# Optimization experiments

Hardware: AMD Instinct MI355X
Metric: run time of the kernel (lower is better)

Reference implementation:

```python
import jax, jax.numpy as jnp
import numpy as np

HID, H, HKV, D, INT, S, T = 2048, 16, 8, 128, 6144, 4096, 512
POS = 0          # absolute position of the first token in this prefill chunk
EPS = 1e-6
SCALE = 1.0 / D ** 0.5
REP = H // HKV


def setup_inputs() -> dict:
    key = jax.random.key(0)
    ks = jax.random.split(key, 12)
    w = lambda k, sh: jax.random.normal(k, sh, dtype=jnp.float32) * 0.02

    hidden_conv = jax.random.normal(ks[0], (1, HID, 1, T), dtype=jnp.float32)

    # RoPE tables for absolute positions POS..POS+T-1, HF half-rotation layout
    inv_freq = 1.0 / (10000.0 ** (jnp.arange(0, D, 2, dtype=jnp.float32) / D))
    pos = (POS + jnp.arange(T, dtype=jnp.float32))
    ang = pos[:, None] * inv_freq[None, :]                      # (T, D/2)
    emb = jnp.concatenate([ang, ang], axis=-1)                  # (T, D)
    cos = jnp.cos(emb)[None]                                    # (1, T, D)
    sin = jnp.sin(emb)[None]

    # one-hot write mask: column t has a 1 at row POS+t
    update_mask = jnp.zeros((S, T), jnp.float32).at[POS + jnp.arange(T), jnp.arange(T)].set(1.0)[None, None]
    # causal mask over the cache: slot s visible to token t iff s <= POS+t
    attn_mask = jnp.where(jnp.arange(S)[None, :] <= (POS + jnp.arange(T))[:, None], 0.0, -1e4).astype(jnp.float32)[None, None]

    k_cache = jnp.zeros((1, HKV, S, D), jnp.float32)
    v_cache = jnp.zeros((1, HKV, S, D), jnp.float32)

    return dict(
        hidden_conv=hidden_conv, cos=cos, sin=sin,
        update_mask=update_mask, attn_mask=attn_mask,
        k_cache=k_cache, v_cache=v_cache,
        wq=w(ks[1], (H * D, HID)), wk=w(ks[2], (HKV * D, HID)),
        wv=w(ks[3], (HKV * D, HID)), wo=w(ks[4], (HID, H * D)),
        ln1_w=jnp.ones((HID,), jnp.float32), ln2_w=jnp.ones((HID,), jnp.float32),
        qn_w=jnp.ones((D,), jnp.float32), kn_w=jnp.ones((D,), jnp.float32),
        w_gate_up=w(ks[5], (2 * INT, HID)), w_down=w(ks[6], (HID, INT)),
    )


def _rms(x, w):
    return x * jax.lax.rsqrt(jnp.mean(x * x, axis=-1, keepdims=True) + EPS) * w


def _rotate_half(x):
    x1, x2 = jnp.split(x, 2, axis=-1)
    return jnp.concatenate([-x2, x1], axis=-1)


def reference(hidden_conv, cos, sin, update_mask, attn_mask, k_cache, v_cache,
              wq, wk, wv, wo, ln1_w, ln2_w, qn_w, kn_w, w_gate_up, w_down):
    # (1, HID, 1, T) conv layout -> (1, T, HID)
    x = jnp.transpose(hidden_conv[:, :, 0, :], (0, 2, 1))

    h = _rms(x, ln1_w)
    # 1x1 conv == linear; channel order h*D+d matches view(1,H,D,T)
    q = jnp.einsum('btc,oc->bto', h, wq).reshape(1, T, H, D).transpose(0, 2, 1, 3)    # (1,H,T,D)
    k = jnp.einsum('btc,oc->bto', h, wk).reshape(1, T, HKV, D).transpose(0, 2, 1, 3)  # (1,HKV,T,D)
    v = jnp.einsum('btc,oc->bto', h, wv).reshape(1, T, HKV, D).transpose(0, 2, 1, 3)

    q = _rms(q, qn_w)
    k = _rms(k, kn_w)

    cos_b = cos[:, None]  # (1,1,T,D)
    sin_b = sin[:, None]
    q = q * cos_b + _rotate_half(q) * sin_b
    k = k * cos_b + _rotate_half(k) * sin_b

    # matmul-based KV cache write via one-hot mask (faithful to original)
    k_inc = jnp.matmul(update_mask, k)                 # (1,HKV,S,D)
    v_inc = jnp.matmul(update_mask, v)
    write_any = jnp.sum(update_mask, axis=-1, keepdims=True)  # (1,1,S,1)
    k_full = k_cache * (1.0 - write_any) + k_inc
    v_full = v_cache * (1.0 - write_any) + v_inc

    k_rep = jnp.repeat(k_full, REP, axis=1)            # (1,H,S,D)
    v_rep = jnp.repeat(v_full, REP, axis=1)

    scores = jnp.einsum('bhtd,bhsd->bhts', q, k_rep) * SCALE + attn_mask  # (1,H,T,S)
    attn = jax.nn.softmax(scores, axis=-1)
    out = jnp.einsum('bhts,bhsd->bhtd', attn, v_rep)   # (1,H,T,D)

    o_in = out.transpose(0, 2, 1, 3).reshape(1, T, H * D)
    attn_out = jnp.einsum('btc,oc->bto', o_in, wo)
    hidden = x + attn_out

    h2 = _rms(hidden, ln2_w)
    gate_up = jnp.einsum('btc,oc->bto', h2, w_gate_up)
    gate, up = jnp.split(gate_up, 2, axis=-1)
    mlp = jnp.einsum('bti,oi->bto', jax.nn.silu(gate) * up, w_down)
    hidden = hidden + mlp

    hidden_out = jnp.transpose(hidden, (0, 2, 1))[:, :, None, :]  # back to (1,HID,1,T)
    return hidden_out, k_full, v_full


if __name__ == '__main__':
    outs = reference(**setup_inputs())
    print([o.shape for o in outs])
```

## Files before the change

### kernel.cpp

```cpp
#include <hip/hip_runtime.h>
#include <hip/hip_bf16.h>
#include <hip/hip_fp16.h>

#define TT 512
#define HIDD 2048
#define NH 16
#define NKV 8
#define DD 128
#define INTR 6144
#define SEQ 4096
#define SCALE 0.08838834764831845f

typedef __attribute__((ext_vector_type(8))) short short8;
typedef __attribute__((ext_vector_type(4))) float floatx4;

static __device__ __forceinline__ unsigned short f2b(float f) {
  unsigned int u = __float_as_uint(f);
  u += 0x7fffu + ((u >> 16) & 1u);
  return (unsigned short)(u >> 16);
}

static __device__ __forceinline__ unsigned int f2b2(float a, float b) {
  __hip_bfloat162 h = __float22bfloat162_rn(make_float2(a, b));
  return *reinterpret_cast<unsigned int*>(&h);
}


static __device__ __forceinline__ void gld16(const void* g, void* l) {
  __builtin_amdgcn_global_load_lds(
      (const __attribute__((address_space(1))) unsigned int*)g,
      (__attribute__((address_space(3))) unsigned int*)l, 16, 0, 0);
}

template <int BM, bool B16>
static __device__ __forceinline__ void stage_tile(const unsigned short* __restrict__ A, int lda,
                                                  const void* __restrict__ B, int ldb, int k0,
                                                  unsigned char* buf, int wave, int lane) {
  {
    const int rpw = BM >> 2;
    const int rl = lane >> 2;
    const int c8 = (((lane & 3) ^ ((rl >> 1) & 3)) << 3);
#pragma unroll
    for (int i = 0; i < BM / 64; ++i) {
      const int rbase = wave * rpw + i * 16;
      gld16(A + (size_t)(rbase + rl) * lda + k0 + c8, buf + (size_t)rbase * 64);
    }
  }
  unsigned char* Bb = buf + BM * 64;
  if constexpr (B16) {
    const unsigned short* Bh = (const unsigned short*)B;
    const int rl = lane >> 2;
    const int c8 = (((lane & 3) ^ ((rl >> 1) & 3)) << 3);
#pragma unroll
    for (int i = 0; i < 2; ++i) {
      const int rbase = wave * 32 + i * 16;
      gld16(Bh + (size_t)(rbase + rl) * ldb + k0 + c8, Bb + (size_t)rbase * 64);
    }
  } else {
    const float* Bf = (const float*)B;
    const int rl = lane >> 3;
    const int sp = lane & 7;
#pragma unroll
    for (int i = 0; i < 4; ++i) {
      const int rbase = wave * 32 + i * 8;
      const int r = rbase + rl;
      gld16(Bf + (size_t)r * ldb + k0 + ((sp ^ (r & 7)) << 2), Bb + (size_t)rbase * 128);
    }
  }
}

template <int BM, bool B16>
static __device__ __forceinline__ void frags_from(const unsigned char* buf, int wr, int wc,
                                                  int lrow, int q,
                                                  short8 (&af)[BM / 32], short8 (&bfr)[4]) {
  const int koffA = ((q ^ ((lrow >> 1) & 3)) << 3);
  const unsigned short* Ab = (const unsigned short*)buf;
#pragma unroll
  for (int mi = 0; mi < BM / 32; ++mi)
    af[mi] = *reinterpret_cast<const short8*>(Ab + (size_t)(wr + mi * 16 + lrow) * 32 + koffA);
  if constexpr (B16) {
    const unsigned short* Bb = (const unsigned short*)(buf + BM * 64);
#pragma unroll
    for (int ni = 0; ni < 4; ++ni)
      bfr[ni] = *reinterpret_cast<const short8*>(Bb + (size_t)(wc + ni * 16 + lrow) * 32 + koffA);
  } else {
    const float* Bf = (const float*)(buf + BM * 64);
    const int s0 = q << 1;
#pragma unroll
    for (int ni = 0; ni < 4; ++ni) {
      const int r = wc + ni * 16 + lrow;
      const float4 x = *reinterpret_cast<const float4*>(Bf + (size_t)r * 32 + ((s0 ^ (r & 7)) << 2));
      const float4 y = *reinterpret_cast<const float4*>(Bf + (size_t)r * 32 + (((s0 + 1) ^ (r & 7)) << 2));
      union { short8 s; unsigned int u[4]; } pk;
      pk.u[0] = f2b2(x.x, x.y); pk.u[1] = f2b2(x.z, x.w);
      pk.u[2] = f2b2(y.x, y.y); pk.u[3] = f2b2(y.z, y.w);
      bfr[ni] = pk.s;
    }
  }
}

template <int BM, bool B16>
static __device__ __forceinline__ void gemm_core(const unsigned short* __restrict__ A, int lda,
                                                 const void* __restrict__ B, int ldb,
                                                 int kbeg, int kend, floatx4 (&acc)[BM / 32][4],
                                                 unsigned char* Ls) {
  constexpr int MI = BM / 32;
  constexpr int TILE = BM * 64 + (B16 ? 8192 : 16384);
  constexpr int NB = (BM / 64) + (B16 ? 2 : 4);
  const int tid = threadIdx.x;
  const int lane = tid & 63, wave = tid >> 6;
  const int wr = (wave >> 1) * (BM >> 1);
  const int wc = (wave & 1) << 6;
  const int lrow = lane & 15;
  const int q = lane >> 4;
  const int NT = (kend - kbeg) >> 5;
  stage_tile<BM, B16>(A, lda, B, ldb, kbeg,      Ls,        wave, lane);
  stage_tile<BM, B16>(A, lda, B, ldb, kbeg + 32, Ls + TILE, wave, lane);
  int p = 0;
  for (int t = 0; t < NT - 1; ++t) {
    if constexpr (NB == 6)      asm volatile("s_waitcnt vmcnt(6)" ::: "memory");
    else if constexpr (NB == 3) asm volatile("s_waitcnt vmcnt(3)" ::: "memory");
    else if constexpr (NB == 4) asm volatile("s_waitcnt vmcnt(4)" ::: "memory");
    else                        asm volatile("s_waitcnt vmcnt(5)" ::: "memory");
    __builtin_amdgcn_sched_barrier(0);
    __builtin_amdgcn_s_barrier();
    short8 af[MI], bfr[4];
    frags_from<BM, B16>(Ls + p * TILE, wr, wc, lrow, q, af, bfr);
    asm volatile("s_waitcnt lgkmcnt(0)" ::: "memory");
    __builtin_amdgcn_sched_barrier(0);
    __builtin_amdgcn_s_barrier();
    if (t + 2 < NT)
      stage_tile<BM, B16>(A, lda, B, ldb, kbeg + (t + 2) * 32, Ls + p * TILE, wave, lane);
#pragma unroll
    for (int mi = 0; mi < MI; ++mi)
#pragma unroll
      for (int ni = 0; ni < 4; ++ni)
        acc[mi][ni] = __builtin_amdgcn_mfma_f32_16x16x32_bf16(af[mi], bfr[ni], acc[mi][ni], 0, 0, 0);
    p ^= 1;
  }
  asm volatile("s_waitcnt vmcnt(0)" ::: "memory");
  __builtin_amdgcn_sched_barrier(0);
  __builtin_amdgcn_s_barrier();
  {
    short8 af[MI], bfr[4];
    frags_from<BM, B16>(Ls + p * TILE, wr, wc, lrow, q, af, bfr);
#pragma unroll
    for (int mi = 0; mi < MI; ++mi)
#pragma unroll
      for (int ni = 0; ni < 4; ++ni)
        acc[mi][ni] = __builtin_amdgcn_mfma_f32_16x16x32_bf16(af[mi], bfr[ni], acc[mi][ni], 0, 0, 0);
  }
}

#define EPI_VARS \
  const int lane = threadIdx.x & 63; \
  const int wave = threadIdx.x >> 6; \
  const int wc = (wave & 1) << 6;    \
  const int lrow = lane & 15;        \
  const int quad = lane >> 4;

#define ZERO_ACC(MI_) \
  floatx4 acc[MI_][4]; \
  _Pragma("unroll") for (int mi = 0; mi < MI_; ++mi) \
  _Pragma("unroll") for (int ni = 0; ni < 4; ++ni) { floatx4 z = {0.f, 0.f, 0.f, 0.f}; acc[mi][ni] = z; }

template <int S>
static __device__ __forceinline__ void swz(int b, int& mt, int& nt, int& s) {
  mt = (b >> 3) & 3;
  const int gid = ((b >> 5) << 3) | (b & 7);
  nt = gid / S;
  s = gid - nt * S;
}


__global__ __launch_bounds__(1024) void k_rms1(const float* __restrict__ conv,
                                               const float* __restrict__ w,
                                               float* __restrict__ xb,
                                               unsigned short* __restrict__ h1b) {
  const int t0 = blockIdx.x << 5;
  const int tid = threadIdx.x;
  const int j = tid & 31;
  const int g = tid >> 5;
  __shared__ float part[32][32];
  __shared__ float tile[32][33];
  __shared__ float rs[32];
  float ss = 0.f;
  for (int c0 = 0; c0 < HIDD; c0 += 32) {
    const float v = conv[(size_t)(c0 + g) * TT + t0 + j];
    ss += v * v;
  }
  part[g][j] = ss;
  __syncthreads();
  if (g == 0) {
    float tot = 0.f;
#pragma unroll
    for (int q = 0; q < 32; ++q) tot += part[q][j];
    rs[j] = rsqrtf(tot * (1.0f / HIDD) + 1e-6f);
  }
  __syncthreads();
  for (int c0 = 0; c0 < HIDD; c0 += 32) {
    tile[g][j] = conv[(size_t)(c0 + g) * TT + t0 + j];
    __syncthreads();
    const float v = tile[j][g];
    const float rv = rs[g];
    xb[(size_t)(t0 + g) * HIDD + c0 + j] = v;
    h1b[(size_t)(t0 + g) * HIDD + c0 + j] = f2b(v * rv * w[c0 + j]);
    __syncthreads();
  }
}

__global__ __launch_bounds__(256) void k_gemm_qkv(const unsigned short* __restrict__ h1b,
                                                  const float* __restrict__ wq,
                                                  const float* __restrict__ wk,
                                                  const float* __restrict__ wv,
                                                  __half* __restrict__ Pq) {
  __shared__ __align__(16) unsigned char Ls[2 * (128 * 64 + 16384)];
  int mt, nt, s;
  swz<4>(blockIdx.x, mt, nt, s);
  const int m0 = mt << 7, n0 = nt << 7;
  const float* Bp;
  if (n0 < 2048)      Bp = wq + (size_t)n0 * HIDD;
  else if (n0 < 3072) Bp = wk + (size_t)(n0 - 2048) * HIDD;
  else                Bp = wv + (size_t)(n0 - 3072) * HIDD;
  ZERO_ACC(4)
  gemm_core<128, false>(h1b + (size_t)m0 * HIDD, HIDD, Bp, HIDD, s * 512, s * 512 + 512, acc, Ls);
  EPI_VARS
  const int wr = (wave >> 1) << 6;
  __half* out = Pq + (size_t)s * (TT * 4096);
#pragma unroll
  for (int mi = 0; mi < 4; ++mi)
#pragma unroll
    for (int ni = 0; ni < 4; ++ni)
#pragma unroll
      for (int rr = 0; rr < 4; ++rr) {
        const int row = m0 + wr + mi * 16 + quad * 4 + rr;
        const int col = n0 + wc + ni * 16 + lrow;
        out[(size_t)row * 4096 + col] = __float2half(acc[mi][ni][rr]);
      }
}

__global__ __launch_bounds__(128) void k_rope(const __half* __restrict__ Pq,
                                              const float* __restrict__ cosb,
                                              const float* __restrict__ sinb,
                                              const float* __restrict__ qnw,
                                              const float* __restrict__ knw,
                                              unsigned short* __restrict__ qb,
                                              unsigned short* __restrict__ kb,
                                              unsigned short* __restrict__ vtb,
                                              float* __restrict__ kout,
                                              float* __restrict__ vout) {
  const int u = blockIdx.x;
  const int t = blockIdx.y;
  const int d = threadIdx.x;
  __shared__ float red[2];
  __shared__ float sh[DD];
  int slot;
  if (u < NH)            slot = u * DD + d;
  else if (u < NH + NKV) slot = 2048 + (u - NH) * DD + d;
  else                   slot = 3072 + (u - NH - NKV) * DD + d;
  const size_t idx = (size_t)t * 4096 + slot;
  float val = __half2float(Pq[idx]) + __half2float(Pq[idx + (size_t)TT * 4096]) +
              __half2float(Pq[idx + 2 * (size_t)TT * 4096]) + __half2float(Pq[idx + 3 * (size_t)TT * 4096]);
  if (u < NH + NKV) {
    float ss = val * val;
    const int lane = d & 63, wid = d >> 6;
#pragma unroll
    for (int o = 32; o; o >>= 1) ss += __shfl_xor(ss, o);
    if (!lane) red[wid] = ss;
    __syncthreads();
    const float r = rsqrtf((red[0] + red[1]) * (1.0f / DD) + 1e-6f);
    const float w = (u < NH) ? qnw[d] : knw[d];
    const float nv = val * r * w;
    sh[d] = nv;
    __syncthreads();
    const float partner = sh[d ^ 64];
    const float rh = (d < 64) ? -partner : partner;
    const float o = nv * cosb[(size_t)t * DD + d] + rh * sinb[(size_t)t * DD + d];
    if (u < NH) {
      qb[(size_t)u * TT * DD + (size_t)t * DD + d] = f2b(o);
    } else {
      const int kh = u - NH;
      kout[(size_t)kh * SEQ * DD + (size_t)t * DD + d] = o;
      kb[(size_t)kh * TT * DD + (size_t)t * DD + d] = f2b(o);
    }
  } else {
    const int vh = u - NH - NKV;
    vout[(size_t)vh * SEQ * DD + (size_t)t * DD + d] = val;
    vtb[(size_t)vh * DD * TT + (size_t)d * TT + t] = f2b(val);
  }
}

__global__ __launch_bounds__(256) void k_tail(const float* __restrict__ kc,
                                              const float* __restrict__ vc,
                                              float* __restrict__ ko,
                                              float* __restrict__ vo) {
  const int i = blockIdx.x * 256 + threadIdx.x;
  const int e = i << 2;
  const int s = (e >> 7) & (SEQ - 1);
  if (s >= TT) {
    reinterpret_cast<float4*>(ko)[i] = reinterpret_cast<const float4*>(kc)[i];
    reinterpret_cast<float4*>(vo)[i] = reinterpret_cast<const float4*>(vc)[i];
  }
}

__global__ __launch_bounds__(256) void k_scores(const unsigned short* __restrict__ qb,
                                                const unsigned short* __restrict__ kb,
                                                float* __restrict__ sc) {
  __shared__ __align__(16) unsigned char Ls[2 * (64 * 64 + 8192)];
  const int m0 = blockIdx.x << 6, n0 = blockIdx.y << 7, h = blockIdx.z;
  ZERO_ACC(2)
  gemm_core<64, true>(qb + (size_t)h * TT * DD + (size_t)m0 * DD, DD,
                      kb + (size_t)(h >> 1) * TT * DD + (size_t)n0 * DD, DD, 0, DD, acc, Ls);
  EPI_VARS
  const int wr = (wave >> 1) << 5;
  float* out = sc + (size_t)h * TT * TT;
#pragma unroll
  for (int mi = 0; mi < 2; ++mi)
#pragma unroll
    for (int ni = 0; ni < 4; ++ni)
#pragma unroll
      for (int rr = 0; rr < 4; ++rr) {
        const int t = m0 + wr + mi * 16 + quad * 4 + rr;
        const int s = n0 + wc + ni * 16 + lrow;
        float v = acc[mi][ni][rr] * SCALE;
        if (s > t) v += -10000.0f;
        out[(size_t)t * TT + s] = v;
      }
}

__global__ __launch_bounds__(256) void k_softmax(const float* __restrict__ sc,
                                                 unsigned short* __restrict__ Pb) {
  const int h = blockIdx.x >> 9, t = blockIdx.x & 511;
  const int tid = threadIdx.x;
  const float* row = sc + ((size_t)h * TT + t) * TT;
  float v0 = row[tid], v1 = row[tid + 256];
  __shared__ float red[4];
  const int lane = tid & 63, wid = tid >> 6;
  float m = fmaxf(v0, v1);
#pragma unroll
  for (int o = 32; o; o >>= 1) m = fmaxf(m, __shfl_xor(m, o));
  if (!lane) red[wid] = m;
  __syncthreads();
  m = fmaxf(fmaxf(red[0], red[1]), fmaxf(red[2], red[3]));
  const float e0 = __expf(v0 - m), e1 = __expf(v1 - m);
  float s = e0 + e1;
  __syncthreads();
#pragma unroll
  for (int o = 32; o; o >>= 1) s += __shfl_xor(s, o);
  if (!lane) red[wid] = s;
  __syncthreads();
  const float inv = 1.0f / (red[0] + red[1] + red[2] + red[3]);
  unsigned short* orow = Pb + ((size_t)h * TT + t) * TT;
  orow[tid] = f2b(e0 * inv);
  orow[tid + 256] = f2b(e1 * inv);
}

__global__ __launch_bounds__(256) void k_pv(const unsigned short* __restrict__ Pb,
                                            const unsigned short* __restrict__ vtb,
                                            float* __restrict__ Ppv) {
  __shared__ __align__(16) unsigned char Ls[2 * (64 * 64 + 8192)];
  const int m0 = blockIdx.x << 6, h = blockIdx.y, s = blockIdx.z;
  ZERO_ACC(2)
  gemm_core<64, true>(Pb + (size_t)h * TT * TT + (size_t)m0 * TT, TT,
                      vtb + (size_t)(h >> 1) * DD * TT, TT, s * 128, s * 128 + 128, acc, Ls);
  EPI_VARS
  const int wr = (wave >> 1) << 5;
  float* out = Ppv + (size_t)s * (TT * HIDD);
#pragma unroll
  for (int mi = 0; mi < 2; ++mi)
#pragma unroll
    for (int ni = 0; ni < 4; ++ni)
#pragma unroll
      for (int rr = 0; rr < 4; ++rr) {
        const int row = m0 + wr + mi * 16 + quad * 4 + rr;
        const int col = wc + ni * 16 + lrow;
        out[(size_t)row * HIDD + h * DD + col] = acc[mi][ni][rr];
      }
}

__global__ __launch_bounds__(256) void k_red_pv(const float* __restrict__ Ppv,
                                                unsigned short* __restrict__ o_inb) {
  const int i = blockIdx.x * 256 + threadIdx.x;
  const float4* p = reinterpret_cast<const float4*>(Ppv);
  float4 a = p[i];
  const float4 b = p[i + 262144], c = p[i + 524288], d = p[i + 786432];
  a.x += b.x + c.x + d.x; a.y += b.y + c.y + d.y;
  a.z += b.z + c.z + d.z; a.w += b.w + c.w + d.w;
  uint2 o;
  o.x = f2b2(a.x, a.y);
  o.y = f2b2(a.z, a.w);
  *reinterpret_cast<uint2*>(o_inb + (size_t)i * 4) = o;
}

__global__ __launch_bounds__(256) void k_gemm_o(const unsigned short* __restrict__ o_inb,
                                                const float* __restrict__ wo,
                                                __half* __restrict__ Po) {
  __shared__ __align__(16) unsigned char Ls[2 * (128 * 64 + 16384)];
  int mt, nt, s;
  swz<16>(blockIdx.x, mt, nt, s);
  const int m0 = mt << 7, n0 = nt << 7;
  ZERO_ACC(4)
  gemm_core<128, false>(o_inb + (size_t)m0 * HIDD, HIDD, wo + (size_t)n0 * HIDD, HIDD,
                        s * 128, s * 128 + 128, acc, Ls);
  EPI_VARS
  const int wr = (wave >> 1) << 6;
  __half* out = Po + (size_t)s * (TT * HIDD);
#pragma unroll
  for (int mi = 0; mi < 4; ++mi)
#pragma unroll
    for (int ni = 0; ni < 4; ++ni)
#pragma unroll
      for (int rr = 0; rr < 4; ++rr) {
        const int row = m0 + wr + mi * 16 + quad * 4 + rr;
        const int col = n0 + wc + ni * 16 + lrow;
        out[(size_t)row * HIDD + col] = __float2half(acc[mi][ni][rr]);
      }
}

__global__ __launch_bounds__(256) void k_rms2(const float* __restrict__ xb,
                                              const __half* __restrict__ Po,
                                              const float* __restrict__ w,
                                              float* __restrict__ hidden,
                                              unsigned short* __restrict__ h2b) {
  const int t = blockIdx.x;
  const int tid = threadIdx.x;
  float2 v[4];
  float ss = 0.f;
#pragma unroll
  for (int i = 0; i < 4; ++i) {
    const int c = (tid << 1) + (i << 9);
    const size_t idx = (size_t)t * HIDD + c;
    float2 a = *reinterpret_cast<const float2*>(xb + idx);
#pragma unroll
    for (int sp = 0; sp < 16; ++sp) {
      const float2 b = __half22float2(*reinterpret_cast<const __half2*>(Po + idx + (size_t)sp * (TT * HIDD)));
      a.x += b.x; a.y += b.y;
    }
    v[i] = a;
    ss += a.x * a.x + a.y * a.y;
  }
  __shared__ float red[4];
  const int lane = tid & 63, wid = tid >> 6;
#pragma unroll
  for (int o = 32; o; o >>= 1) ss += __shfl_xor(ss, o);
  if (!lane) red[wid] = ss;
  __syncthreads();
  const float tot = red[0] + red[1] + red[2] + red[3];
  const float r = rsqrtf(tot * (1.0f / HIDD) + 1e-6f);
#pragma unroll
  for (int i = 0; i < 4; ++i) {
    const int c = (tid << 1) + (i << 9);
    const size_t idx = (size_t)t * HIDD + c;
    *reinterpret_cast<float2*>(hidden + idx) = v[i];
    const float2 wv2 = *reinterpret_cast<const float2*>(w + c);
    *reinterpret_cast<unsigned int*>(h2b + idx) = f2b2(v[i].x * r * wv2.x, v[i].y * r * wv2.y);
  }
}

__global__ __launch_bounds__(256) void k_gemm_gu(const unsigned short* __restrict__ h2b,
                                                 const float* __restrict__ wgu,
                                                 __half* __restrict__ guh) {
  __shared__ __align__(16) unsigned char Ls[2 * (128 * 64 + 16384)];
  int mt, nt, s;
  swz<2>(blockIdx.x, mt, nt, s);
  const int m0 = mt << 7, n0 = nt << 7;
  ZERO_ACC(4)
  gemm_core<128, false>(h2b + (size_t)m0 * HIDD, HIDD, wgu + (size_t)n0 * HIDD, HIDD,
                        s * 1024, s * 1024 + 1024, acc, Ls);
  EPI_VARS
  const int wr = (wave >> 1) << 6;
  __half* out = guh + (size_t)s * (TT * 2 * INTR);
#pragma unroll
  for (int mi = 0; mi < 4; ++mi)
#pragma unroll
    for (int ni = 0; ni < 4; ++ni)
#pragma unroll
      for (int rr = 0; rr < 4; ++rr) {
        const int row = m0 + wr + mi * 16 + quad * 4 + rr;
        const int col = n0 + wc + ni * 16 + lrow;
        out[(size_t)row * (2 * INTR) + col] = __float2half(acc[mi][ni][rr]);
      }
}

__global__ __launch_bounds__(256) void k_silu(const __half* __restrict__ guh,
                                              unsigned short* __restrict__ actb) {
  const int j0 = (blockIdx.x * 256 + threadIdx.x) << 1;
  const int t = blockIdx.y;
  const size_t base = (size_t)t * (2 * INTR) + j0;
  const size_t off = (size_t)TT * (2 * INTR);
  const float2 g0 = __half22float2(*reinterpret_cast<const __half2*>(guh + base));
  const float2 g1 = __half22float2(*reinterpret_cast<const __half2*>(guh + off + base));
  const float2 u0 = __half22float2(*reinterpret_cast<const __half2*>(guh + base + INTR));
  const float2 u1 = __half22float2(*reinterpret_cast<const __half2*>(guh + off + base + INTR));
  const float gx = g0.x + g1.x, gy = g0.y + g1.y;
  const float ux = u0.x + u1.x, uy = u0.y + u1.y;
  const float a0 = gx / (1.f + __expf(-gx)) * ux;
  const float a1 = gy / (1.f + __expf(-gy)) * uy;
  *reinterpret_cast<unsigned int*>(actb + (size_t)t * INTR + j0) = f2b2(a0, a1);
}

__global__ __launch_bounds__(256) void k_gemm_down(const unsigned short* __restrict__ actb,
                                                   const float* __restrict__ wdn,
                                                   __half* __restrict__ Pdn) {
  __shared__ __align__(16) unsigned char Ls[2 * (128 * 64 + 16384)];
  int mt, nt, s;
  swz<12>(blockIdx.x, mt, nt, s);
  const int m0 = mt << 7, n0 = nt << 7;
  ZERO_ACC(4)
  gemm_core<128, false>(actb + (size_t)m0 * INTR, INTR, wdn + (size_t)n0 * INTR, INTR,
                        s * 512, s * 512 + 512, acc, Ls);
  EPI_VARS
  const int wr = (wave >> 1) << 6;
  __half* out = Pdn + (size_t)s * (TT * HIDD);
#pragma unroll
  for (int mi = 0; mi < 4; ++mi)
#pragma unroll
    for (int ni = 0; ni < 4; ++ni)
#pragma unroll
      for (int rr = 0; rr < 4; ++rr) {
        const int row = m0 + wr + mi * 16 + quad * 4 + rr;
        const int col = n0 + wc + ni * 16 + lrow;
        out[(size_t)row * HIDD + col] = __float2half(acc[mi][ni][rr]);
      }
}

__global__ __launch_bounds__(256) void k_final(const float* __restrict__ hidden,
                                               const __half* __restrict__ Pdn,
                                               float* __restrict__ out0) {
  __shared__ float tile[32][33];
  const int c0 = blockIdx.x << 5, t0 = blockIdx.y << 5;
  const int tx = threadIdx.x & 31, ty0 = (threadIdx.x >> 5) << 2;
#pragma unroll
  for (int i = 0; i < 4; ++i) {
    const int t = t0 + ty0 + i;
    const size_t idx = (size_t)t * HIDD + c0 + tx;
    float a = hidden[idx];
#pragma unroll
    for (int sp = 0; sp < 12; ++sp) a += __half2float(Pdn[idx + (size_t)sp * (TT * HIDD)]);
    tile[ty0 + i][tx] = a;
  }
  __syncthreads();
#pragma unroll
  for (int i = 0; i < 4; ++i)
    out0[(size_t)(c0 + ty0 + i) * TT + t0 + tx] = tile[tx][ty0 + i];
}

extern "C" void kernel_launch(void* const* d_in, const int* in_sizes, int n_in,
                              void* d_out, int out_size, void* d_ws, size_t ws_size,
                              hipStream_t stream) {
  const float* conv   = (const float*)d_in[0];
  const float* cosb   = (const float*)d_in[1];
  const float* sinb   = (const float*)d_in[2];
  const float* kcache = (const float*)d_in[5];
  const float* vcache = (const float*)d_in[6];
  const float* wq  = (const float*)d_in[7];
  const float* wk  = (const float*)d_in[8];
  const float* wv  = (const float*)d_in[9];
  const float* wo  = (const float*)d_in[10];
  const float* ln1 = (const float*)d_in[11];
  const float* ln2 = (const float*)d_in[12];
  const float* qnw = (const float*)d_in[13];
  const float* knw = (const float*)d_in[14];
  const float* wgu = (const float*)d_in[15];
  const float* wdn = (const float*)d_in[16];

  float* ws = (float*)d_ws;
  float* xb = ws + 0;
  unsigned short* h1b  = (unsigned short*)(ws + 1048576);
  unsigned short* o_inb = h1b;
  unsigned short* h2b  = (unsigned short*)(ws + 1572864);
  float* hidden = ws + 2097152;
  unsigned short* qb  = (unsigned short*)(ws + 3145728);
  unsigned short* kb  = qb + 1048576;
  unsigned short* vtb = kb + 524288;
  unsigned short* actb = (unsigned short*)(ws + 4194304);
  float* R   = ws + 5767168;
  __half* Pqh = (__half*)R;
  unsigned short* Pb = (unsigned short*)R;
  float* sc  = R + 2097152;
  float* Ppv = R + 2097152;
  __half* Poh = (__half*)R;
  __half* guh = (__half*)R;
  __half* Pdnh = (__half*)R;

  float* out0 = (float*)d_out;
  float* kout = out0 + 1048576;
  float* vout = kout + 4194304;

  k_rms1<<<16, 1024, 0, stream>>>(conv, ln1, xb, h1b);
  k_gemm_qkv<<<512, 256, 0, stream>>>(h1b, wq, wk, wv, Pqh);
  k_rope<<<dim3(NH + 2 * NKV, TT), 128, 0, stream>>>(Pqh, cosb, sinb, qnw, knw, qb, kb, vtb, kout, vout);
  k_tail<<<4096, 256, 0, stream>>>(kcache, vcache, kout, vout);
  k_scores<<<dim3(8, 4, NH), 256, 0, stream>>>(qb, kb, sc);
  k_softmax<<<NH * TT, 256, 0, stream>>>(sc, Pb);
  k_pv<<<dim3(8, NH, 4), 256, 0, stream>>>(Pb, vtb, Ppv);
  k_red_pv<<<1024, 256, 0, stream>>>(Ppv, o_inb);
  k_gemm_o<<<1024, 256, 0, stream>>>(o_inb, wo, Poh);
  k_rms2<<<TT, 256, 0, stream>>>(xb, Poh, ln2, hidden, h2b);
  k_gemm_gu<<<768, 256, 0, stream>>>(h2b, wgu, guh);
  k_silu<<<dim3(12, TT), 256, 0, stream>>>(guh, actb);
  k_gemm_down<<<768, 256, 0, stream>>>(actb, wdn, Pdnh);
  k_final<<<dim3(HIDD / 32, TT / 32), 256, 0, stream>>>(hidden, Pdnh, out0);
}
```

Measured before the change: 470.7 us.

## Skip masked attention tiles, fuse cache tail copy, halve O-proj split-K

Score and PV GEMM tiles lying entirely above the causal diagonal are now skipped, and softmax treats masked entries as -inf without reading them. The KV-cache tail copy moves into extra blocks of the softmax launch, which removes one kernel launch. The O-projection split-K factor drops from 16 to 8, halving the fp16 partials that rms2 must sum. The XOR LDS swizzle in the GEMM staging and fragment loads is removed, so bank conflicts on LDS reads may rise.

New measurement: 459.0 us. 2.5% less time.

```diff
diff --git a/kernel.cpp b/kernel.cpp
--- a/kernel.cpp
+++ b/kernel.cpp
@@ -39,7 +39,7 @@
   {
     const int rpw = BM >> 2;
     const int rl = lane >> 2;
-    const int c8 = (((lane & 3) ^ ((rl >> 1) & 3)) << 3);
+    const int c8 = (lane & 3) << 3;
 #pragma unroll
     for (int i = 0; i < BM / 64; ++i) {
       const int rbase = wave * rpw + i * 16;
@@ -50,7 +50,7 @@
   if constexpr (B16) {
     const unsigned short* Bh = (const unsigned short*)B;
     const int rl = lane >> 2;
-    const int c8 = (((lane & 3) ^ ((rl >> 1) & 3)) << 3);
+    const int c8 = (lane & 3) << 3;
 #pragma unroll
     for (int i = 0; i < 2; ++i) {
       const int rbase = wave * 32 + i * 16;
@@ -71,21 +71,20 @@
 
 template <int BM, bool B16>
 static __device__ __forceinline__ void frags_from(const unsigned char* buf, int wr, int wc,
-                                                  int lrow, int q,
+                                                  int lrow, int koff,
                                                   short8 (&af)[BM / 32], short8 (&bfr)[4]) {
-  const int koffA = ((q ^ ((lrow >> 1) & 3)) << 3);
   const unsigned short* Ab = (const unsigned short*)buf;
 #pragma unroll
   for (int mi = 0; mi < BM / 32; ++mi)
-    af[mi] = *reinterpret_cast<const short8*>(Ab + (size_t)(wr + mi * 16 + lrow) * 32 + koffA);
+    af[mi] = *reinterpret_cast<const short8*>(Ab + (size_t)(wr + mi * 16 + lrow) * 32 + koff);
   if constexpr (B16) {
     const unsigned short* Bb = (const unsigned short*)(buf + BM * 64);
 #pragma unroll
     for (int ni = 0; ni < 4; ++ni)
-      bfr[ni] = *reinterpret_cast<const short8*>(Bb + (size_t)(wc + ni * 16 + lrow) * 32 + koffA);
+      bfr[ni] = *reinterpret_cast<const short8*>(Bb + (size_t)(wc + ni * 16 + lrow) * 32 + koff);
   } else {
     const float* Bf = (const float*)(buf + BM * 64);
-    const int s0 = q << 1;
+    const int s0 = koff >> 2;
 #pragma unroll
     for (int ni = 0; ni < 4; ++ni) {
       const int r = wc + ni * 16 + lrow;
@@ -112,7 +111,7 @@
   const int wr = (wave >> 1) * (BM >> 1);
   const int wc = (wave & 1) << 6;
   const int lrow = lane & 15;
-  const int q = lane >> 4;
+  const int koff = (lane >> 4) << 3;
   const int NT = (kend - kbeg) >> 5;
   stage_tile<BM, B16>(A, lda, B, ldb, kbeg,      Ls,        wave, lane);
   stage_tile<BM, B16>(A, lda, B, ldb, kbeg + 32, Ls + TILE, wave, lane);
@@ -125,7 +124,7 @@
     __builtin_amdgcn_sched_barrier(0);
     __builtin_amdgcn_s_barrier();
     short8 af[MI], bfr[4];
-    frags_from<BM, B16>(Ls + p * TILE, wr, wc, lrow, q, af, bfr);
+    frags_from<BM, B16>(Ls + p * TILE, wr, wc, lrow, koff, af, bfr);
     asm volatile("s_waitcnt lgkmcnt(0)" ::: "memory");
     __builtin_amdgcn_sched_barrier(0);
     __builtin_amdgcn_s_barrier();
@@ -143,7 +142,7 @@
   __builtin_amdgcn_s_barrier();
   {
     short8 af[MI], bfr[4];
-    frags_from<BM, B16>(Ls + p * TILE, wr, wc, lrow, q, af, bfr);
+    frags_from<BM, B16>(Ls + p * TILE, wr, wc, lrow, koff, af, bfr);
 #pragma unroll
     for (int mi = 0; mi < MI; ++mi)
 #pragma unroll
@@ -290,24 +289,12 @@
   }
 }
 
-__global__ __launch_bounds__(256) void k_tail(const float* __restrict__ kc,
-                                              const float* __restrict__ vc,
-                                              float* __restrict__ ko,
-                                              float* __restrict__ vo) {
-  const int i = blockIdx.x * 256 + threadIdx.x;
-  const int e = i << 2;
-  const int s = (e >> 7) & (SEQ - 1);
-  if (s >= TT) {
-    reinterpret_cast<float4*>(ko)[i] = reinterpret_cast<const float4*>(kc)[i];
-    reinterpret_cast<float4*>(vo)[i] = reinterpret_cast<const float4*>(vc)[i];
-  }
-}
-
 __global__ __launch_bounds__(256) void k_scores(const unsigned short* __restrict__ qb,
                                                 const unsigned short* __restrict__ kb,
                                                 float* __restrict__ sc) {
+  const int m0 = blockIdx.x << 6, n0 = blockIdx.y << 7, h = blockIdx.z;
+  if (n0 >= m0 + 64) return;
   __shared__ __align__(16) unsigned char Ls[2 * (64 * 64 + 8192)];
-  const int m0 = blockIdx.x << 6, n0 = blockIdx.y << 7, h = blockIdx.z;
   ZERO_ACC(2)
   gemm_core<64, true>(qb + (size_t)h * TT * DD + (size_t)m0 * DD, DD,
                       kb + (size_t)(h >> 1) * TT * DD + (size_t)n0 * DD, DD, 0, DD, acc, Ls);
@@ -329,11 +316,27 @@
 }
 
 __global__ __launch_bounds__(256) void k_softmax(const float* __restrict__ sc,
-                                                 unsigned short* __restrict__ Pb) {
-  const int h = blockIdx.x >> 9, t = blockIdx.x & 511;
+                                                 unsigned short* __restrict__ Pb,
+                                                 const float* __restrict__ kc,
+                                                 const float* __restrict__ vc,
+                                                 float* __restrict__ ko,
+                                                 float* __restrict__ vo) {
+  const int bid = blockIdx.x;
   const int tid = threadIdx.x;
+  if (bid >= NH * TT) {
+    const int i = (bid - NH * TT) * 256 + tid;
+    const int e = i << 2;
+    const int s = (e >> 7) & (SEQ - 1);
+    if (s >= TT) {
+      reinterpret_cast<float4*>(ko)[i] = reinterpret_cast<const float4*>(kc)[i];
+      reinterpret_cast<float4*>(vo)[i] = reinterpret_cast<const float4*>(vc)[i];
+    }
+    return;
+  }
+  const int h = bid >> 9, t = bid & 511;
   const float* row = sc + ((size_t)h * TT + t) * TT;
-  float v0 = row[tid], v1 = row[tid + 256];
+  float v0 = (tid <= t) ? row[tid] : -1e30f;
+  float v1 = (tid + 256 <= t) ? row[tid + 256] : -1e30f;
   __shared__ float red[4];
   const int lane = tid & 63, wid = tid >> 6;
   float m = fmaxf(v0, v1);
@@ -361,8 +364,9 @@
   __shared__ __align__(16) unsigned char Ls[2 * (64 * 64 + 8192)];
   const int m0 = blockIdx.x << 6, h = blockIdx.y, s = blockIdx.z;
   ZERO_ACC(2)
-  gemm_core<64, true>(Pb + (size_t)h * TT * TT + (size_t)m0 * TT, TT,
-                      vtb + (size_t)(h >> 1) * DD * TT, TT, s * 128, s * 128 + 128, acc, Ls);
+  if (s * 128 <= m0 + 63)
+    gemm_core<64, true>(Pb + (size_t)h * TT * TT + (size_t)m0 * TT, TT,
+                        vtb + (size_t)(h >> 1) * DD * TT, TT, s * 128, s * 128 + 128, acc, Ls);
   EPI_VARS
   const int wr = (wave >> 1) << 5;
   float* out = Ppv + (size_t)s * (TT * HIDD);
@@ -397,11 +401,11 @@
                                                 __half* __restrict__ Po) {
   __shared__ __align__(16) unsigned char Ls[2 * (128 * 64 + 16384)];
   int mt, nt, s;
-  swz<16>(blockIdx.x, mt, nt, s);
+  swz<8>(blockIdx.x, mt, nt, s);
   const int m0 = mt << 7, n0 = nt << 7;
   ZERO_ACC(4)
   gemm_core<128, false>(o_inb + (size_t)m0 * HIDD, HIDD, wo + (size_t)n0 * HIDD, HIDD,
-                        s * 128, s * 128 + 128, acc, Ls);
+                        s * 256, s * 256 + 256, acc, Ls);
   EPI_VARS
   const int wr = (wave >> 1) << 6;
   __half* out = Po + (size_t)s * (TT * HIDD);
@@ -432,7 +436,7 @@
     const size_t idx = (size_t)t * HIDD + c;
     float2 a = *reinterpret_cast<const float2*>(xb + idx);
 #pragma unroll
-    for (int sp = 0; sp < 16; ++sp) {
+    for (int sp = 0; sp < 8; ++sp) {
       const float2 b = __half22float2(*reinterpret_cast<const __half2*>(Po + idx + (size_t)sp * (TT * HIDD)));
       a.x += b.x; a.y += b.y;
     }
@@ -590,12 +594,11 @@
   k_rms1<<<16, 1024, 0, stream>>>(conv, ln1, xb, h1b);
   k_gemm_qkv<<<512, 256, 0, stream>>>(h1b, wq, wk, wv, Pqh);
   k_rope<<<dim3(NH + 2 * NKV, TT), 128, 0, stream>>>(Pqh, cosb, sinb, qnw, knw, qb, kb, vtb, kout, vout);
-  k_tail<<<4096, 256, 0, stream>>>(kcache, vcache, kout, vout);
   k_scores<<<dim3(8, 4, NH), 256, 0, stream>>>(qb, kb, sc);
-  k_softmax<<<NH * TT, 256, 0, stream>>>(sc, Pb);
+  k_softmax<<<NH * TT + 4096, 256, 0, stream>>>(sc, Pb, kcache, vcache, kout, vout);
   k_pv<<<dim3(8, NH, 4), 256, 0, stream>>>(Pb, vtb, Ppv);
   k_red_pv<<<1024, 256, 0, stream>>>(Ppv, o_inb);
-  k_gemm_o<<<1024, 256, 0, stream>>>(o_inb, wo, Poh);
+  k_gemm_o<<<512, 256, 0, stream>>>(o_inb, wo, Poh);
   k_rms2<<<TT, 256, 0, stream>>>(xb, Poh, ln2, hidden, h2b);
   k_gemm_gu<<<768, 256, 0, stream>>>(h2b, wgu, guh);
   k_silu<<<dim3(12, TT), 256, 0, stream>>>(guh, actb);
```
